# Performance work log

Hardware: AMD Instinct MI355X
Metric: run time of the kernel (lower is better)

Reference implementation:

```python
import jax, jax.numpy as jnp
import numpy as np


def setup_inputs() -> dict:
    key = jax.random.key(0)
    k1, k2 = jax.random.split(key)
    qs = jax.random.normal(k1, (8, 4096, 1024), dtype=jnp.float32)      # [B, L, D]
    memory = jax.random.normal(k2, (512, 1024), dtype=jnp.float32)       # [M, D]
    return {"qs": qs, "memory": memory}


def reference(qs, memory):
    # s = qs @ memory.T  -> [B, L, M]; permute -> [B, M, L]
    s = jnp.einsum("bld,md->bml", qs, memory)
    # softmax over L (last dim after permute)
    v = jax.nn.softmax(s, axis=2)                 # [B, M, L]
    # r = v @ qs -> [B, M, D]
    r = jnp.einsum("bml,bld->bmd", v, qs)
    return (r, memory)
```

## Files before the change

### kernel.cpp

```cpp
#include <hip/hip_runtime.h>
#include <hip/hip_fp16.h>


#define B_ 8
#define L_ 4096
#define D_ 1024
#define M_ 512

typedef _Float16 halfT;
typedef _Float16 half8 __attribute__((ext_vector_type(8)));
typedef _Float16 half4_t __attribute__((ext_vector_type(4)));
typedef float f32x4 __attribute__((ext_vector_type(4)));

#define OFF_MEM16 0ull
#define SZ_MEM16  (512ull*1024*2)
#define OFF_QS16  (OFF_MEM16 + SZ_MEM16)
#define SZ_QS16   (8ull*4096*1024*2)
#define OFF_S     (OFF_QS16 + SZ_QS16)
#define SZ_S      (8ull*512*4096*4)
#define OFF_P16   (OFF_S + SZ_S)
#define SZ_P16    (8ull*512*4096*2)
#define OFF_INVL  (OFF_P16 + SZ_P16)
#define SZ_INVL   (8ull*512*4)
#define OFF_MLOC  (OFF_INVL + SZ_INVL)
#define SZ_MLOC   (8ull*16*512*4)
#define WS_NEED   (OFF_MLOC + SZ_MLOC)
#define OFF_RP    OFF_S

#define SWZ(n) ((((n)&7) ^ (((n)>>5)&7)))

__device__ __forceinline__ void gload_lds16(const halfT* g, halfT* l) {
  __builtin_amdgcn_global_load_lds(
      (const __attribute__((address_space(1))) unsigned int*)(const void*)g,
      (__attribute__((address_space(3))) unsigned int*)l, 16, 0, 0);
}

__global__ __launch_bounds__(256)
void prep_all(const float* __restrict__ qs, const float* __restrict__ mem,
              halfT* __restrict__ q16, halfT* __restrict__ mem16) {
  int bid = blockIdx.x;
  int tid = threadIdx.x;
  if (bid < 2048) {
    size_t base = (size_t)bid*256 + tid;
    #pragma unroll
    for (int it = 0; it < 8; ++it) {
      size_t i8 = base + (size_t)it*524288;
      size_t row = i8 >> 7;
      int c = (int)(i8 & 127);
      int kt = c >> 3, g = c & 7;
      const float* src = qs + i8*8;
      f32x4 x0 = *(const f32x4*)&src[0];
      f32x4 x1 = *(const f32x4*)&src[4];
      half8 h;
      #pragma unroll
      for (int j = 0; j < 4; ++j) { h[j] = (halfT)x0[j]; h[4+j] = (halfT)x1[j]; }
      *(half8*)&q16[row*1024 + kt*64 + ((g ^ ((int)row & 7)) << 3)] = h;
    }
  } else {
    int i8 = (bid - 2048)*256 + tid;
    int row = i8 >> 7, c = i8 & 127;
    int kt = c >> 3, g = c & 7;
    const float* src = mem + (size_t)i8*8;
    f32x4 x0 = *(const f32x4*)src;
    f32x4 x1 = *(const f32x4*)(src + 4);
    half8 h;
    #pragma unroll
    for (int j = 0; j < 4; ++j) { h[j] = (halfT)x0[j]; h[4+j] = (halfT)x1[j]; }
    *(half8*)&mem16[(size_t)row*1024 + kt*64 + ((g ^ (row & 7)) << 3)] = h;
  }
}

__global__ __launch_bounds__(512, 2)
void gemm_qk(const halfT* __restrict__ mem16, const halfT* __restrict__ qs16,
             halfT* __restrict__ S16, float* __restrict__ mloc)
{
  __shared__ __attribute__((aligned(16))) halfT At[2][256*64];
  __shared__ __attribute__((aligned(16))) halfT Bt[2][256*64];

  int bid = blockIdx.x;
  int swz = (bid & 7)*32 + (bid >> 3);
  int b   = swz >> 5;
  int rem = swz & 31;
  int nt  = rem >> 1;
  int mt  = rem & 1;

  int tid = threadIdx.x;
  int w = tid >> 6, lane = tid & 63, lg = lane >> 4, li = lane & 15;
  int wm = w >> 2, wn = w & 3;
  int sl = li & 7;
  int rA = tid >> 3;
  int cA = (tid & 7)*8;

  const halfT* Ab = mem16 + (size_t)mt*256*1024;
  const halfT* Bb = qs16 + ((size_t)b*L_ + nt*256)*D_;

  f32x4 acc[8][4];
  #pragma unroll
  for (int i=0;i<8;++i)
    #pragma unroll
    for (int j=0;j<4;++j) acc[i][j] = (f32x4){0.f,0.f,0.f,0.f};

#define STAGE_QK(nb_, kt_)                                                     \
  do {                                                                         \
    const halfT* a0 = Ab + (size_t)(kt_)*64 + cA;                              \
    const halfT* b0 = Bb + (size_t)(kt_)*64 + cA;                              \
    _Pragma("unroll")                                                          \
    for (int j = 0; j < 4; ++j) {                                              \
      int r = rA + j*64;                                                       \
      gload_lds16(a0 + (size_t)r*1024, &At[nb_][(tid + j*512)*8]);             \
      gload_lds16(b0 + (size_t)r*1024, &Bt[nb_][(tid + j*512)*8]);             \
    }                                                                          \
  } while (0)

#define COMPUTE_QK(nb_)                                                        \
  do {                                                                         \
    _Pragma("unroll")                                                          \
    for (int ksub = 0; ksub < 2; ++ksub) {                                     \
      int gx = ((ksub*4 + lg) ^ sl) << 3;                                      \
      half8 Af[8], Bf[4];                                                      \
      _Pragma("unroll")                                                        \
      for (int mf = 0; mf < 8; ++mf)                                           \
        Af[mf] = *(const half8*)&At[nb_][(wm*128 + mf*16 + li)*64 + gx];       \
      _Pragma("unroll")                                                        \
      for (int nf = 0; nf < 4; ++nf)                                           \
        Bf[nf] = *(const half8*)&Bt[nb_][(wn*64 + nf*16 + li)*64 + gx];        \
      _Pragma("unroll")                                                        \
      for (int mf = 0; mf < 8; ++mf)                                           \
        _Pragma("unroll")                                                      \
        for (int nf = 0; nf < 4; ++nf)                                         \
          acc[mf][nf] = __builtin_amdgcn_mfma_f32_16x16x32_f16(Af[mf], Bf[nf], acc[mf][nf], 0,0,0); \
    }                                                                          \
  } while (0)

  STAGE_QK(0, 0);
  STAGE_QK(1, 1);
  asm volatile("s_waitcnt vmcnt(8)" ::: "memory");
  __builtin_amdgcn_sched_barrier(0);
  __builtin_amdgcn_s_barrier();

  for (int kt = 0; kt < 16; ++kt) {
    COMPUTE_QK(kt & 1);
    __builtin_amdgcn_s_barrier();
    if (kt + 2 < 16) {
      STAGE_QK(kt & 1, kt + 2);
      asm volatile("s_waitcnt vmcnt(8) lgkmcnt(0)" ::: "memory");
    } else {
      asm volatile("s_waitcnt vmcnt(0) lgkmcnt(0)" ::: "memory");
    }
    __builtin_amdgcn_sched_barrier(0);
    __builtin_amdgcn_s_barrier();
  }
#undef STAGE_QK
#undef COMPUTE_QK

  float* red = (float*)&At[0][0];
  float m4[8][4];
  #pragma unroll
  for (int mf = 0; mf < 8; ++mf)
    #pragma unroll
    for (int r = 0; r < 4; ++r) {
      float vmax = fmaxf(fmaxf(acc[mf][0][r], acc[mf][1][r]),
                         fmaxf(acc[mf][2][r], acc[mf][3][r]));
      #pragma unroll
      for (int off = 1; off < 16; off <<= 1) vmax = fmaxf(vmax, __shfl_xor(vmax, off));
      if (li == 0) red[w*128 + mf*16 + lg*4 + r] = vmax;
    }
  __syncthreads();
  #pragma unroll
  for (int mf = 0; mf < 8; ++mf)
    #pragma unroll
    for (int r = 0; r < 4; ++r) {
      int idx = mf*16 + lg*4 + r;
      m4[mf][r] = fmaxf(fmaxf(red[(wm*4+0)*128 + idx], red[(wm*4+1)*128 + idx]),
                        fmaxf(red[(wm*4+2)*128 + idx], red[(wm*4+3)*128 + idx]));
    }
  if (wn == 0 && li == 0) {
    #pragma unroll
    for (int mf = 0; mf < 8; ++mf)
      #pragma unroll
      for (int r = 0; r < 4; ++r) {
        int m = mt*256 + wm*128 + mf*16 + lg*4 + r;
        mloc[((size_t)b*16 + nt)*M_ + m] = m4[mf][r];
      }
  }
  halfT* Cb = S16 + (size_t)b*M_*L_;
  int cpb = nt*256 + wn*64 + li*4;
  #pragma unroll
  for (int mf = 0; mf < 8; ++mf) {
    #pragma unroll
    for (int r = 0; r < 4; ++r) {
      int row = mt*256 + wm*128 + mf*16 + lg*4 + r;
      half4_t hv;
      #pragma unroll
      for (int nf = 0; nf < 4; ++nf) hv[nf] = (halfT)(acc[mf][nf][r] - m4[mf][r]);
      *(half4_t*)&Cb[(size_t)row*L_ + cpb] = hv;
    }
  }
}

__global__ __launch_bounds__(512, 2)
void gemm_pv(const halfT* __restrict__ P16, const halfT* __restrict__ qs16,
             halfT* __restrict__ rp16)
{
  __shared__ __attribute__((aligned(16))) halfT At[2][256*64];
  __shared__ __attribute__((aligned(16))) halfT Bt[2][256*64];

  int bid = blockIdx.x;
  int swz = (bid & 7)*32 + (bid >> 3);
  int ks  = swz >> 6;
  int rem = swz & 63;
  int b   = rem >> 3;
  int nt  = (rem >> 1) & 3;
  int mt  = rem & 1;

  int tid = threadIdx.x;
  int w = tid >> 6, lane = tid & 63, lg = lane >> 4, li = lane & 15;
  int wm = w >> 2, wn = w & 3;
  int sl = li & 7;

  const halfT* Ab = P16 + (size_t)b*M_*L_ + (size_t)mt*256*L_ + ks*1024;
  const halfT* Bb = qs16 + ((size_t)b*L_ + ks*1024)*D_ + nt*256;
  int krow = tid >> 3;
  int seg  = tid & 7;
  int pinv = ((krow & 3) << 4) | (krow >> 2);
  int rs   = pinv & 7;

  f32x4 acc[8][4];
  #pragma unroll
  for (int i=0;i<8;++i)
    #pragma unroll
    for (int j=0;j<4;++j) acc[i][j] = (f32x4){0.f,0.f,0.f,0.f};

  half8 hx[4];

#define GLOADB_PV(kt_)                                                         \
  do {                                                                         \
    const halfT* rowp = Bb + (size_t)((kt_)*64 + pinv)*D_ + (seg >> 1)*64;     \
    _Pragma("unroll")                                                          \
    for (int j = 0; j < 4; ++j)                                                \
      hx[j] = *(const half8*)(rowp + ((((seg & 1)*4 + j) ^ rs) << 3));         \
  } while (0)

#define STAGEA_PV(nb_, kt_)                                                    \
  do {                                                                         \
    const halfT* a0 = Ab + (size_t)(kt_)*64 + (tid & 7)*8;                     \
    _Pragma("unroll")                                                          \
    for (int j = 0; j < 4; ++j)                                                \
      gload_lds16(a0 + (size_t)((tid >> 3) + j*64)*L_, &At[nb_][(tid + j*512)*8]); \
  } while (0)

#define WRITEB_PV(nb_)                                                         \
  do {                                                                         \
    _Pragma("unroll")                                                          \
    for (int i = 0; i < 32; ++i) {                                             \
      int n_ = seg*32 + i;                                                     \
      Bt[nb_][n_*64 + ((((krow >> 3) ^ SWZ(n_)) << 3)) + (krow & 7)] =         \
          hx[i >> 3][i & 7];                                                   \
    }                                                                          \
  } while (0)

#define COMPUTE_PV(nb_)                                                        \
  do {                                                                         \
    _Pragma("unroll")                                                          \
    for (int ksub = 0; ksub < 2; ++ksub) {                                     \
      int gx = ((ksub*4 + lg) ^ sl) << 3;                                      \
      half8 Af[8], Bf[4];                                                      \
      _Pragma("unroll")                                                        \
      for (int mf = 0; mf < 8; ++mf)                                           \
        Af[mf] = *(const half8*)&At[nb_][(wm*128 + mf*16 + li)*64 + gx];       \
      _Pragma("unroll")                                                        \
      for (int nf = 0; nf < 4; ++nf) {                                         \
        int n_ = wn*64 + nf*16 + li;                                           \
        Bf[nf] = *(const half8*)&Bt[nb_][n_*64 + (((ksub*4 + lg) ^ SWZ(n_)) << 3)]; \
      }                                                                        \
      _Pragma("unroll")                                                        \
      for (int mf = 0; mf < 8; ++mf)                                           \
        _Pragma("unroll")                                                      \
        for (int nf = 0; nf < 4; ++nf)                                         \
          acc[mf][nf] = __builtin_amdgcn_mfma_f32_16x16x32_f16(Af[mf], Bf[nf], acc[mf][nf], 0,0,0); \
    }                                                                          \
  } while (0)

  GLOADB_PV(0);
  STAGEA_PV(0, 0);
  STAGEA_PV(1, 1);
  WRITEB_PV(0);
  GLOADB_PV(1);
  asm volatile("s_waitcnt vmcnt(8) lgkmcnt(0)" ::: "memory");
  __builtin_amdgcn_sched_barrier(0);
  __builtin_amdgcn_s_barrier();

  for (int kt = 0; kt < 16; ++kt) {
    COMPUTE_PV(kt & 1);
    __builtin_amdgcn_s_barrier();
    if (kt + 1 < 16) WRITEB_PV((kt + 1) & 1);
    if (kt + 2 < 16) {
      GLOADB_PV(kt + 2);
      STAGEA_PV(kt & 1, kt + 2);
      asm volatile("s_waitcnt vmcnt(8) lgkmcnt(0)" ::: "memory");
    } else {
      asm volatile("s_waitcnt vmcnt(0) lgkmcnt(0)" ::: "memory");
    }
    __builtin_amdgcn_sched_barrier(0);
    __builtin_amdgcn_s_barrier();
  }
#undef GLOADB_PV
#undef STAGEA_PV
#undef WRITEB_PV
#undef COMPUTE_PV

  halfT* Cb = rp16 + (size_t)ks*((size_t)B_*M_*D_) + (size_t)b*M_*D_;
  int cpbase = nt*256 + wn*64 + li*4;
  #pragma unroll
  for (int mf = 0; mf < 8; ++mf) {
    #pragma unroll
    for (int r = 0; r < 4; ++r) {
      int row = mt*256 + wm*128 + mf*16 + lg*4 + r;
      half4_t hv;
      #pragma unroll
      for (int nf = 0; nf < 4; ++nf) hv[nf] = (halfT)acc[mf][nf][r];
      *(half4_t*)&Cb[(size_t)row*D_ + cpbase] = hv;
    }
  }
}

__global__ __launch_bounds__(256)
void softmax_rows(const halfT* __restrict__ S16, const float* __restrict__ mloc,
                  halfT* __restrict__ P, float* __restrict__ invl)
{
  int tid = threadIdx.x;
  int w = tid >> 6, lane = tid & 63;
  int row = blockIdx.x*4 + w;
  int b = row >> 9, m = row & 511;
  int rs  = row & 7;
  float mv = (lane < 16) ? mloc[((size_t)b*16 + lane)*M_ + m] : -3.0e38f;
  float M = mv;
  #pragma unroll
  for (int off = 1; off < 64; off <<= 1) M = fmaxf(M, __shfl_xor(M, off));

  const halfT* src = S16 + (size_t)row*L_;
  halfT* dst = P + (size_t)row*L_;
  float sum = 0.f;
  #pragma unroll
  for (int i = 0; i < 16; ++i) {
    float di = __shfl(mv, i) - M;
    half4_t s4 = *(const half4_t*)&src[(size_t)(i*64 + lane)*4];
    half4_t h;
    #pragma unroll
    for (int e = 0; e < 4; ++e) {
      float ev = __expf((float)s4[e] + di);
      sum += ev;
      h[e] = (halfT)ev;
    }
    int c = i*64 + lane;
    int kt = c >> 4, g = (c >> 1) & 7, o = c & 1;
    *(half4_t*)&dst[kt*64 + ((g ^ rs) << 3) + o*4] = h;
  }
  #pragma unroll
  for (int off = 1; off < 64; off <<= 1) sum += __shfl_xor(sum, off);
  if (lane == 0) invl[row] = 1.0f / sum;
}

__global__ __launch_bounds__(256)
void combine_scale(const halfT* __restrict__ rp16, const float* __restrict__ invl,
                   float* __restrict__ out)
{
  int bm = blockIdx.x;
  int t = threadIdx.x;
  size_t off = (size_t)bm*D_ + t*4;
  f32x4 v = (f32x4){0.f,0.f,0.f,0.f};
  #pragma unroll
  for (int s = 0; s < 4; ++s) {
    half4_t h = *(const half4_t*)&rp16[(size_t)s*((size_t)B_*M_*D_) + off];
    #pragma unroll
    for (int j = 0; j < 4; ++j) v[j] += (float)h[j];
  }
  float sc = invl[bm];
  v *= sc;
  int W = (t >> 4) << 6;
  float* ob = out + (size_t)bm*D_;
  #pragma unroll
  for (int j = 0; j < 4; ++j)
    ob[W + j*16 + (t & 15)] = v[j];
}

__global__ void fallback_kernel(const float* __restrict__ qs,
                                const float* __restrict__ mem,
                                float* __restrict__ out)
{
  __shared__ float w_lds[4][4096];
  __shared__ float mem_s[4][1024];
  __shared__ float redb[256];
  int blk = blockIdx.x;
  int b = blk >> 7;
  int m0 = (blk & 127)*4;
  int tid = threadIdx.x;

  for (int i = tid; i < 4*1024; i += 256)
    mem_s[i>>10][i&1023] = mem[(size_t)(m0 + (i>>10))*D_ + (i&1023)];
  __syncthreads();

  float mx[4] = {-3e38f,-3e38f,-3e38f,-3e38f};
  for (int l = tid; l < L_; l += 256) {
    const float* qp = qs + ((size_t)b*L_ + l)*D_;
    float dot[4] = {0,0,0,0};
    for (int dd = 0; dd < D_; dd += 4) {
      f32x4 qv = *(const f32x4*)(qp + dd);
      #pragma unroll
      for (int mi=0; mi<4; ++mi)
        dot[mi] += qv[0]*mem_s[mi][dd] + qv[1]*mem_s[mi][dd+1]
                 + qv[2]*mem_s[mi][dd+2] + qv[3]*mem_s[mi][dd+3];
    }
    #pragma unroll
    for (int mi=0; mi<4; ++mi) { w_lds[mi][l] = dot[mi]; mx[mi] = fmaxf(mx[mi], dot[mi]); }
  }
  float Mv[4], Zv[4];
  for (int mi=0; mi<4; ++mi) {
    redb[tid] = mx[mi]; __syncthreads();
    for (int s=128; s>0; s>>=1) { if (tid<s) redb[tid]=fmaxf(redb[tid],redb[tid+s]); __syncthreads(); }
    Mv[mi] = redb[0]; __syncthreads();
  }
  float sm[4] = {0,0,0,0};
  for (int l = tid; l < L_; l += 256)
    #pragma unroll
    for (int mi=0; mi<4; ++mi) {
      float wv = __expf(w_lds[mi][l] - Mv[mi]);
      w_lds[mi][l] = wv; sm[mi] += wv;
    }
  for (int mi=0; mi<4; ++mi) {
    redb[tid] = sm[mi]; __syncthreads();
    for (int s=128; s>0; s>>=1) { if (tid<s) redb[tid]+=redb[tid+s]; __syncthreads(); }
    Zv[mi] = redb[0]; __syncthreads();
  }
  int d0 = tid*4;
  f32x4 a[4];
  #pragma unroll
  for (int mi=0;mi<4;++mi) a[mi] = (f32x4){0,0,0,0};
  for (int l = 0; l < L_; ++l) {
    f32x4 qv = *(const f32x4*)(qs + ((size_t)b*L_ + l)*D_ + d0);
    #pragma unroll
    for (int mi=0; mi<4; ++mi) a[mi] += qv * w_lds[mi][l];
  }
  #pragma unroll
  for (int mi=0; mi<4; ++mi) {
    float invz = 1.f/Zv[mi];
    #pragma unroll
    for (int c=0; c<4; ++c)
      out[((size_t)b*M_ + m0 + mi)*D_ + d0 + c] = a[mi][c]*invz;
  }
}

extern "C" void kernel_launch(void* const* d_in, const int* in_sizes, int n_in,
                              void* d_out, int out_size, void* d_ws, size_t ws_size,
                              hipStream_t stream) {
  const float* qs  = (const float*)d_in[0];
  const float* mem = (const float*)d_in[1];
  float* out = (float*)d_out;

  hipMemcpyAsync(out + (size_t)B_*M_*D_, mem, (size_t)M_*D_*sizeof(float),
                 hipMemcpyDeviceToDevice, stream);

  if (ws_size >= (size_t)WS_NEED) {
    char* base = (char*)d_ws;
    halfT* mem16 = (halfT*)(base + OFF_MEM16);
    halfT* qs16  = (halfT*)(base + OFF_QS16);
    halfT* S16   = (halfT*)(base + OFF_S);
    halfT* P16   = (halfT*)(base + OFF_P16);
    float* invl  = (float*)(base + OFF_INVL);
    float* mloc  = (float*)(base + OFF_MLOC);
    halfT* rp16  = (halfT*)(base + OFF_RP);

    prep_all<<<2304, 256, 0, stream>>>(qs, mem, qs16, mem16);
    gemm_qk<<<256, 512, 0, stream>>>(mem16, qs16, S16, mloc);
    softmax_rows<<<1024, 256, 0, stream>>>(S16, mloc, P16, invl);
    gemm_pv<<<256, 512, 0, stream>>>(P16, qs16, rp16);
    combine_scale<<<4096, 256, 0, stream>>>(rp16, invl, out);
  } else {
    fallback_kernel<<<1024, 256, 0, stream>>>(qs, mem, out);
  }
}
```

Measured before the change: 144.9 us.

## Overlap global prefetch with MFMA by preloading LDS fragments before barrier

In both the QK and PV GEMM main loops, the A (and for QK also B) fragments for the whole k-tile are read from LDS into registers first. A barrier follows, then the next-stage global-to-LDS loads are issued, and the MFMAs run while those loads are in flight. Before, the loads were issued only after all MFMAs finished. The aim is to hide global load latency behind matrix compute. The cost is more register pressure from holding two k-subtiles of fragments, and in PV the B writes now happen in the other buffer during compute.

```diff
diff --git a/kernel.cpp b/kernel.cpp
--- a/kernel.cpp
+++ b/kernel.cpp
@@ -112,26 +112,6 @@
     }                                                                          \
   } while (0)
 
-#define COMPUTE_QK(nb_)                                                        \
-  do {                                                                         \
-    _Pragma("unroll")                                                          \
-    for (int ksub = 0; ksub < 2; ++ksub) {                                     \
-      int gx = ((ksub*4 + lg) ^ sl) << 3;                                      \
-      half8 Af[8], Bf[4];                                                      \
-      _Pragma("unroll")                                                        \
-      for (int mf = 0; mf < 8; ++mf)                                           \
-        Af[mf] = *(const half8*)&At[nb_][(wm*128 + mf*16 + li)*64 + gx];       \
-      _Pragma("unroll")                                                        \
-      for (int nf = 0; nf < 4; ++nf)                                           \
-        Bf[nf] = *(const half8*)&Bt[nb_][(wn*64 + nf*16 + li)*64 + gx];        \
-      _Pragma("unroll")                                                        \
-      for (int mf = 0; mf < 8; ++mf)                                           \
-        _Pragma("unroll")                                                      \
-        for (int nf = 0; nf < 4; ++nf)                                         \
-          acc[mf][nf] = __builtin_amdgcn_mfma_f32_16x16x32_f16(Af[mf], Bf[nf], acc[mf][nf], 0,0,0); \
-    }                                                                          \
-  } while (0)
-
   STAGE_QK(0, 0);
   STAGE_QK(1, 1);
   asm volatile("s_waitcnt vmcnt(8)" ::: "memory");
@@ -139,19 +119,35 @@
   __builtin_amdgcn_s_barrier();
 
   for (int kt = 0; kt < 16; ++kt) {
-    COMPUTE_QK(kt & 1);
-    __builtin_amdgcn_s_barrier();
-    if (kt + 2 < 16) {
-      STAGE_QK(kt & 1, kt + 2);
-      asm volatile("s_waitcnt vmcnt(8) lgkmcnt(0)" ::: "memory");
-    } else {
-      asm volatile("s_waitcnt vmcnt(0) lgkmcnt(0)" ::: "memory");
-    }
+    int nb = kt & 1;
+    half8 Af[2][8], Bf[2][4];
+    #pragma unroll
+    for (int ksub = 0; ksub < 2; ++ksub) {
+      int gx = ((ksub*4 + lg) ^ sl) << 3;
+      #pragma unroll
+      for (int mf = 0; mf < 8; ++mf)
+        Af[ksub][mf] = *(const half8*)&At[nb][(wm*128 + mf*16 + li)*64 + gx];
+      #pragma unroll
+      for (int nf = 0; nf < 4; ++nf)
+        Bf[ksub][nf] = *(const half8*)&Bt[nb][(wn*64 + nf*16 + li)*64 + gx];
+    }
+    asm volatile("s_waitcnt lgkmcnt(0)" ::: "memory");
     __builtin_amdgcn_sched_barrier(0);
     __builtin_amdgcn_s_barrier();
+    if (kt + 2 < 16) STAGE_QK(nb, kt + 2);
+    #pragma unroll
+    for (int ksub = 0; ksub < 2; ++ksub)
+      #pragma unroll
+      for (int mf = 0; mf < 8; ++mf)
+        #pragma unroll
+        for (int nf = 0; nf < 4; ++nf)
+          acc[mf][nf] = __builtin_amdgcn_mfma_f32_16x16x32_f16(Af[ksub][mf], Bf[ksub][nf], acc[mf][nf], 0,0,0);
+    if (kt + 2 < 16) asm volatile("s_waitcnt vmcnt(8)" ::: "memory");
+    else             asm volatile("s_waitcnt vmcnt(0)" ::: "memory");
+    __builtin_amdgcn_sched_barrier(0);
+    __builtin_amdgcn_s_barrier();
   }
 #undef STAGE_QK
-#undef COMPUTE_QK
 
   float* red = (float*)&At[0][0];
   float m4[8][4];
@@ -259,28 +255,6 @@
     }                                                                          \
   } while (0)
 
-#define COMPUTE_PV(nb_)                                                        \
-  do {                                                                         \
-    _Pragma("unroll")                                                          \
-    for (int ksub = 0; ksub < 2; ++ksub) {                                     \
-      int gx = ((ksub*4 + lg) ^ sl) << 3;                                      \
-      half8 Af[8], Bf[4];                                                      \
-      _Pragma("unroll")                                                        \
-      for (int mf = 0; mf < 8; ++mf)                                           \
-        Af[mf] = *(const half8*)&At[nb_][(wm*128 + mf*16 + li)*64 + gx];       \
-      _Pragma("unroll")                                                        \
-      for (int nf = 0; nf < 4; ++nf) {                                         \
-        int n_ = wn*64 + nf*16 + li;                                           \
-        Bf[nf] = *(const half8*)&Bt[nb_][n_*64 + (((ksub*4 + lg) ^ SWZ(n_)) << 3)]; \
-      }                                                                        \
-      _Pragma("unroll")                                                        \
-      for (int mf = 0; mf < 8; ++mf)                                           \
-        _Pragma("unroll")                                                      \
-        for (int nf = 0; nf < 4; ++nf)                                         \
-          acc[mf][nf] = __builtin_amdgcn_mfma_f32_16x16x32_f16(Af[mf], Bf[nf], acc[mf][nf], 0,0,0); \
-    }                                                                          \
-  } while (0)
-
   GLOADB_PV(0);
   STAGEA_PV(0, 0);
   STAGEA_PV(1, 1);
@@ -291,23 +265,44 @@
   __builtin_amdgcn_s_barrier();
 
   for (int kt = 0; kt < 16; ++kt) {
-    COMPUTE_PV(kt & 1);
+    int nb = kt & 1;
+    half8 As[2][8];
+    #pragma unroll
+    for (int ksub = 0; ksub < 2; ++ksub) {
+      int gx = ((ksub*4 + lg) ^ sl) << 3;
+      #pragma unroll
+      for (int mf = 0; mf < 8; ++mf)
+        As[ksub][mf] = *(const half8*)&At[nb][(wm*128 + mf*16 + li)*64 + gx];
+    }
+    asm volatile("s_waitcnt lgkmcnt(0)" ::: "memory");
+    __builtin_amdgcn_sched_barrier(0);
     __builtin_amdgcn_s_barrier();
-    if (kt + 1 < 16) WRITEB_PV((kt + 1) & 1);
-    if (kt + 2 < 16) {
-      GLOADB_PV(kt + 2);
-      STAGEA_PV(kt & 1, kt + 2);
-      asm volatile("s_waitcnt vmcnt(8) lgkmcnt(0)" ::: "memory");
-    } else {
-      asm volatile("s_waitcnt vmcnt(0) lgkmcnt(0)" ::: "memory");
-    }
+    if (kt + 1 < 16) WRITEB_PV(nb ^ 1);
+    if (kt + 2 < 16) { GLOADB_PV(kt + 2); STAGEA_PV(nb, kt + 2); }
+    #pragma unroll
+    for (int ksub = 0; ksub < 2; ++ksub) {
+      int gx = ((ksub*4 + lg) ^ sl) << 3;
+      (void)gx;
+      half8 Bf[4];
+      #pragma unroll
+      for (int nf = 0; nf < 4; ++nf) {
+        int n_ = wn*64 + nf*16 + li;
+        Bf[nf] = *(const half8*)&Bt[nb][n_*64 + (((ksub*4 + lg) ^ SWZ(n_)) << 3)];
+      }
+      #pragma unroll
+      for (int mf = 0; mf < 8; ++mf)
+        #pragma unroll
+        for (int nf = 0; nf < 4; ++nf)
+          acc[mf][nf] = __builtin_amdgcn_mfma_f32_16x16x32_f16(As[ksub][mf], Bf[nf], acc[mf][nf], 0,0,0);
+    }
+    if (kt + 2 < 16) asm volatile("s_waitcnt vmcnt(8) lgkmcnt(0)" ::: "memory");
+    else             asm volatile("s_waitcnt vmcnt(0) lgkmcnt(0)" ::: "memory");
     __builtin_amdgcn_sched_barrier(0);
     __builtin_amdgcn_s_barrier();
   }
 #undef GLOADB_PV
 #undef STAGEA_PV
 #undef WRITEB_PV
-#undef COMPUTE_PV
 
   halfT* Cb = rp16 + (size_t)ks*((size_t)B_*M_*D_) + (size_t)b*M_*D_;
   int cpbase = nt*256 + wn*64 + li*4;
```

After: 146.7 us. About the same (+1.2%).

## Fuse softmax exponentiation into PV GEMM operand load, drop softmax pass

Applied to the files above, without the earlier changes.

Removes the standalone softmax kernel. The QK GEMM now also emits per-tile partial exp-sums, a tiny stats kernel combines tile maxima and sums into a row max and inverse normaliser, and the PV GEMM reads the max-subtracted scores and exponentiates them while staging the A operand into LDS. This avoids one full read and write of the 8x512x4096 half-precision score matrix. In exchange the PV kernel does its A loads through registers instead of direct global-to-LDS loads and adds exp work to its inner loop, which may hurt its pipelining.

```diff
diff --git a/kernel.cpp b/kernel.cpp
--- a/kernel.cpp
+++ b/kernel.cpp
@@ -18,14 +18,17 @@
 #define SZ_QS16   (8ull*4096*1024*2)
 #define OFF_S     (OFF_QS16 + SZ_QS16)
 #define SZ_S      (8ull*512*4096*4)
-#define OFF_P16   (OFF_S + SZ_S)
-#define SZ_P16    (8ull*512*4096*2)
-#define OFF_INVL  (OFF_P16 + SZ_P16)
+#define OFF_RP    (OFF_S + SZ_S)
+#define SZ_RP     (8ull*512*4096*2)
+#define OFF_INVL  (OFF_RP + SZ_RP)
 #define SZ_INVL   (8ull*512*4)
 #define OFF_MLOC  (OFF_INVL + SZ_INVL)
 #define SZ_MLOC   (8ull*16*512*4)
-#define WS_NEED   (OFF_MLOC + SZ_MLOC)
-#define OFF_RP    OFF_S
+#define OFF_ZLOC  (OFF_MLOC + SZ_MLOC)
+#define SZ_ZLOC   (8ull*16*512*4)
+#define OFF_MROW  (OFF_ZLOC + SZ_ZLOC)
+#define SZ_MROW   (8ull*512*4)
+#define WS_NEED   (OFF_MROW + SZ_MROW)
 
 #define SWZ(n) ((((n)&7) ^ (((n)>>5)&7)))
 
@@ -72,7 +75,8 @@
 
 __global__ __launch_bounds__(512, 2)
 void gemm_qk(const halfT* __restrict__ mem16, const halfT* __restrict__ qs16,
-             halfT* __restrict__ S16, float* __restrict__ mloc)
+             halfT* __restrict__ S16, float* __restrict__ mloc,
+             float* __restrict__ zloc)
 {
   __shared__ __attribute__((aligned(16))) halfT At[2][256*64];
   __shared__ __attribute__((aligned(16))) halfT Bt[2][256*64];
@@ -153,7 +157,8 @@
 #undef STAGE_QK
 #undef COMPUTE_QK
 
-  float* red = (float*)&At[0][0];
+  float* red  = (float*)&At[0][0];
+  float* red2 = red + 1024;
   float m4[8][4];
   #pragma unroll
   for (int mf = 0; mf < 8; ++mf)
@@ -174,13 +179,29 @@
       m4[mf][r] = fmaxf(fmaxf(red[(wm*4+0)*128 + idx], red[(wm*4+1)*128 + idx]),
                         fmaxf(red[(wm*4+2)*128 + idx], red[(wm*4+3)*128 + idx]));
     }
+  #pragma unroll
+  for (int mf = 0; mf < 8; ++mf)
+    #pragma unroll
+    for (int r = 0; r < 4; ++r) {
+      float e = 0.f;
+      #pragma unroll
+      for (int nf = 0; nf < 4; ++nf) e += __expf(acc[mf][nf][r] - m4[mf][r]);
+      #pragma unroll
+      for (int off = 1; off < 16; off <<= 1) e += __shfl_xor(e, off);
+      if (li == 0) red2[w*128 + mf*16 + lg*4 + r] = e;
+    }
+  __syncthreads();
   if (wn == 0 && li == 0) {
     #pragma unroll
     for (int mf = 0; mf < 8; ++mf)
       #pragma unroll
       for (int r = 0; r < 4; ++r) {
-        int m = mt*256 + wm*128 + mf*16 + lg*4 + r;
+        int idx = mf*16 + lg*4 + r;
+        int m = mt*256 + wm*128 + idx;
+        float z = red2[(wm*4+0)*128 + idx] + red2[(wm*4+1)*128 + idx]
+                + red2[(wm*4+2)*128 + idx] + red2[(wm*4+3)*128 + idx];
         mloc[((size_t)b*16 + nt)*M_ + m] = m4[mf][r];
+        zloc[((size_t)b*16 + nt)*M_ + m] = z;
       }
   }
   halfT* Cb = S16 + (size_t)b*M_*L_;
@@ -198,8 +219,27 @@
   }
 }
 
+__global__ __launch_bounds__(256)
+void stats_rows(const float* __restrict__ mloc, const float* __restrict__ zloc,
+                float* __restrict__ Mrow, float* __restrict__ invl)
+{
+  int row = blockIdx.x*256 + threadIdx.x;
+  int b = row >> 9, m = row & 511;
+  const float* mp = mloc + (size_t)b*16*M_ + m;
+  const float* zp = zloc + (size_t)b*16*M_ + m;
+  float ml[16], M = -3.0e38f;
+  #pragma unroll
+  for (int t = 0; t < 16; ++t) { ml[t] = mp[(size_t)t*M_]; M = fmaxf(M, ml[t]); }
+  float Z = 0.f;
+  #pragma unroll
+  for (int t = 0; t < 16; ++t) Z += zp[(size_t)t*M_] * __expf(ml[t] - M);
+  Mrow[row] = M;
+  invl[row] = 1.0f / Z;
+}
+
 __global__ __launch_bounds__(512, 2)
-void gemm_pv(const halfT* __restrict__ P16, const halfT* __restrict__ qs16,
+void gemm_pv(const halfT* __restrict__ S16, const halfT* __restrict__ qs16,
+             const float* __restrict__ mloc, const float* __restrict__ Mrow,
              halfT* __restrict__ rp16)
 {
   __shared__ __attribute__((aligned(16))) halfT At[2][256*64];
@@ -218,12 +258,24 @@
   int wm = w >> 2, wn = w & 3;
   int sl = li & 7;
 
-  const halfT* Ab = P16 + (size_t)b*M_*L_ + (size_t)mt*256*L_ + ks*1024;
+  const halfT* Ab = S16 + (size_t)b*M_*L_ + (size_t)mt*256*L_ + ks*1024;
   const halfT* Bb = qs16 + ((size_t)b*L_ + ks*1024)*D_ + nt*256;
   int krow = tid >> 3;
   int seg  = tid & 7;
   int pinv = ((krow & 3) << 4) | (krow >> 2);
   int rs   = pinv & 7;
+  int r0   = tid >> 3;
+  int rsA  = r0 & 7;
+
+  float dl[4][4];
+  #pragma unroll
+  for (int j = 0; j < 4; ++j) {
+    int m = mt*256 + r0 + j*64;
+    float Mr = Mrow[b*512 + m];
+    #pragma unroll
+    for (int t = 0; t < 4; ++t)
+      dl[j][t] = mloc[((size_t)b*16 + ks*4 + t)*M_ + m] - Mr;
+  }
 
   f32x4 acc[8][4];
   #pragma unroll
@@ -231,7 +283,27 @@
     #pragma unroll
     for (int j=0;j<4;++j) acc[i][j] = (f32x4){0.f,0.f,0.f,0.f};
 
-  half8 hx[4];
+  half8 ax[4], hx[4];
+
+#define GLOADA_PV(kt_)                                                         \
+  do {                                                                         \
+    _Pragma("unroll")                                                          \
+    for (int j = 0; j < 4; ++j)                                                \
+      ax[j] = *(const half8*)(Ab + (size_t)(r0 + j*64)*L_ + (kt_)*64 + seg*8); \
+  } while (0)
+
+#define WRITEA_PV(nb_, kt_)                                                    \
+  do {                                                                         \
+    int t_ = (kt_) >> 2;                                                       \
+    _Pragma("unroll")                                                          \
+    for (int j = 0; j < 4; ++j) {                                              \
+      half8 h;                                                                 \
+      _Pragma("unroll")                                                        \
+      for (int e = 0; e < 8; ++e)                                              \
+        h[e] = (halfT)__expf((float)ax[j][e] + dl[j][t_]);                     \
+      *(half8*)&At[nb_][(r0 + j*64)*64 + ((seg ^ rsA) << 3)] = h;              \
+    }                                                                          \
+  } while (0)
 
 #define GLOADB_PV(kt_)                                                         \
   do {                                                                         \
@@ -239,14 +311,6 @@
     _Pragma("unroll")                                                          \
     for (int j = 0; j < 4; ++j)                                                \
       hx[j] = *(const half8*)(rowp + ((((seg & 1)*4 + j) ^ rs) << 3));         \
-  } while (0)
-
-#define STAGEA_PV(nb_, kt_)                                                    \
-  do {                                                                         \
-    const halfT* a0 = Ab + (size_t)(kt_)*64 + (tid & 7)*8;                     \
-    _Pragma("unroll")                                                          \
-    for (int j = 0; j < 4; ++j)                                                \
-      gload_lds16(a0 + (size_t)((tid >> 3) + j*64)*L_, &At[nb_][(tid + j*512)*8]); \
   } while (0)
 
 #define WRITEB_PV(nb_)                                                         \
@@ -281,31 +345,26 @@
     }                                                                          \
   } while (0)
 
-  GLOADB_PV(0);
-  STAGEA_PV(0, 0);
-  STAGEA_PV(1, 1);
-  WRITEB_PV(0);
-  GLOADB_PV(1);
-  asm volatile("s_waitcnt vmcnt(8) lgkmcnt(0)" ::: "memory");
+  GLOADA_PV(0); GLOADB_PV(0);
+  WRITEA_PV(0, 0); WRITEB_PV(0);
+  GLOADA_PV(1); GLOADB_PV(1);
+  asm volatile("s_waitcnt lgkmcnt(0)" ::: "memory");
   __builtin_amdgcn_sched_barrier(0);
   __builtin_amdgcn_s_barrier();
 
   for (int kt = 0; kt < 16; ++kt) {
-    COMPUTE_PV(kt & 1);
+    int nb = kt & 1;
+    COMPUTE_PV(nb);
     __builtin_amdgcn_s_barrier();
-    if (kt + 1 < 16) WRITEB_PV((kt + 1) & 1);
-    if (kt + 2 < 16) {
-      GLOADB_PV(kt + 2);
-      STAGEA_PV(kt & 1, kt + 2);
-      asm volatile("s_waitcnt vmcnt(8) lgkmcnt(0)" ::: "memory");
-    } else {
-      asm volatile("s_waitcnt vmcnt(0) lgkmcnt(0)" ::: "memory");
-    }
+    if (kt + 1 < 16) { WRITEA_PV(nb ^ 1, kt + 1); WRITEB_PV(nb ^ 1); }
+    if (kt + 2 < 16) { GLOADA_PV(kt + 2); GLOADB_PV(kt + 2); }
+    asm volatile("s_waitcnt lgkmcnt(0)" ::: "memory");
     __builtin_amdgcn_sched_barrier(0);
     __builtin_amdgcn_s_barrier();
   }
+#undef GLOADA_PV
+#undef WRITEA_PV
 #undef GLOADB_PV
-#undef STAGEA_PV
 #undef WRITEB_PV
 #undef COMPUTE_PV
 
@@ -322,43 +381,6 @@
       *(half4_t*)&Cb[(size_t)row*D_ + cpbase] = hv;
     }
   }
-}
-
-__global__ __launch_bounds__(256)
-void softmax_rows(const halfT* __restrict__ S16, const float* __restrict__ mloc,
-                  halfT* __restrict__ P, float* __restrict__ invl)
-{
-  int tid = threadIdx.x;
-  int w = tid >> 6, lane = tid & 63;
-  int row = blockIdx.x*4 + w;
-  int b = row >> 9, m = row & 511;
-  int rs  = row & 7;
-  float mv = (lane < 16) ? mloc[((size_t)b*16 + lane)*M_ + m] : -3.0e38f;
-  float M = mv;
-  #pragma unroll
-  for (int off = 1; off < 64; off <<= 1) M = fmaxf(M, __shfl_xor(M, off));
-
-  const halfT* src = S16 + (size_t)row*L_;
-  halfT* dst = P + (size_t)row*L_;
-  float sum = 0.f;
-  #pragma unroll
-  for (int i = 0; i < 16; ++i) {
-    float di = __shfl(mv, i) - M;
-    half4_t s4 = *(const half4_t*)&src[(size_t)(i*64 + lane)*4];
-    half4_t h;
-    #pragma unroll
-    for (int e = 0; e < 4; ++e) {
-      float ev = __expf((float)s4[e] + di);
-      sum += ev;
-      h[e] = (halfT)ev;
-    }
-    int c = i*64 + lane;
-    int kt = c >> 4, g = (c >> 1) & 7, o = c & 1;
-    *(half4_t*)&dst[kt*64 + ((g ^ rs) << 3) + o*4] = h;
-  }
-  #pragma unroll
-  for (int off = 1; off < 64; off <<= 1) sum += __shfl_xor(sum, off);
-  if (lane == 0) invl[row] = 1.0f / sum;
 }
 
 __global__ __launch_bounds__(256)
@@ -465,15 +487,16 @@
     halfT* mem16 = (halfT*)(base + OFF_MEM16);
     halfT* qs16  = (halfT*)(base + OFF_QS16);
     halfT* S16   = (halfT*)(base + OFF_S);
-    halfT* P16   = (halfT*)(base + OFF_P16);
+    halfT* rp16  = (halfT*)(base + OFF_RP);
     float* invl  = (float*)(base + OFF_INVL);
     float* mloc  = (float*)(base + OFF_MLOC);
-    halfT* rp16  = (halfT*)(base + OFF_RP);
+    float* zloc  = (float*)(base + OFF_ZLOC);
+    float* Mrow  = (float*)(base + OFF_MROW);
 
     prep_all<<<2304, 256, 0, stream>>>(qs, mem, qs16, mem16);
-    gemm_qk<<<256, 512, 0, stream>>>(mem16, qs16, S16, mloc);
-    softmax_rows<<<1024, 256, 0, stream>>>(S16, mloc, P16, invl);
-    gemm_pv<<<256, 512, 0, stream>>>(P16, qs16, rp16);
+    gemm_qk<<<256, 512, 0, stream>>>(mem16, qs16, S16, mloc, zloc);
+    stats_rows<<<16, 256, 0, stream>>>(mloc, zloc, Mrow, invl);
+    gemm_pv<<<256, 512, 0, stream>>>(S16, qs16, mloc, Mrow, rp16);
     combine_scale<<<4096, 256, 0, stream>>>(rp16, invl, out);
   } else {
     fallback_kernel<<<1024, 256, 0, stream>>>(qs, mem, out);
```

Measured after the change: 157.2 us. +8.5%, slower.
